# Optimization experiments

Hardware: AMD Instinct MI355X
Metric: run time of the kernel (lower is better)

## Reference

```python
import jax, jax.numpy as jnp
import numpy as np
from jax import lax

EPS = 1e-12  # torch F.normalize eps

def setup_inputs() -> dict:
    key = jax.random.key(0)
    k1, k2, k3, k4, k5 = jax.random.split(key, 5)
    N = 4194304
    L = 64
    return {
        "T": jax.random.normal(k1, (1,), dtype=jnp.float32),
        "closed_manifold": jax.random.normal(k2, (N, 2), dtype=jnp.float32),
        "Ws": jax.random.normal(k3, (L, 2, 2), dtype=jnp.float32) * 0.5,
        "bs": jax.random.normal(k4, (L, 2), dtype=jnp.float32) * 0.1,
        "final_W": jax.random.normal(k5, (2, 2), dtype=jnp.float32) * 0.5,
    }

def reference(T, closed_manifold, Ws, bs, final_W):
    # T is accepted but unused, exactly as in the original forward.
    def step(X, wb):
        W, b = wb                      # W: [2,2], b: [2]
        Y = X @ W.T + b                # linear: [N,2]
        A = jnp.tanh(Y)                # activation
        X = (A + Y) * 0.5              # residual averaging (skip_connections=True)
        return X, None
    X, _ = lax.scan(step, closed_manifold, (Ws, bs))
    X = X @ final_W.T                  # final bias-free linear
    # F.normalize(X, p=2, dim=1): row-wise unit vectors with eps clamp
    norm = jnp.sqrt(jnp.sum(X * X, axis=-1, keepdims=True))
    X = X / jnp.maximum(norm, EPS)
    return X
```

## Files before the change

### kernel.cpp

```cpp
#include <hip/hip_runtime.h>


#define KPT 8
#define BLOCK 256

__global__ __launch_bounds__(BLOCK) void nig_kernel(
    const float* __restrict__ X_in,
    const float* __restrict__ Ws,
    const float* __restrict__ bs,
    const float* __restrict__ fW,
    float* __restrict__ out,
    int M,
    int L)
{
    const int tid = blockIdx.x * blockDim.x + threadIdx.x;
    const int nthreads = gridDim.x * blockDim.x;

    const float4* __restrict__ in4 = (const float4*)X_in;
    float4* __restrict__ out4 = (float4*)out;

    float x0[KPT], x1[KPT];
    int idx4[KPT / 2];
    bool ok[KPT / 2];

    #pragma unroll
    for (int j = 0; j < KPT / 2; ++j) {
        idx4[j] = tid + j * nthreads;
        ok[j] = idx4[j] < M;
        float4 v = ok[j] ? in4[idx4[j]] : make_float4(0.f, 0.f, 0.f, 0.f);
        x0[2 * j]     = v.x; x1[2 * j]     = v.y;
        x0[2 * j + 1] = v.z; x1[2 * j + 1] = v.w;
    }

    const float C = 2.8853900817779268f;

    for (int l = 0; l < L; ++l) {
        const float4 w = ((const float4*)Ws)[l];
        const float2 b = ((const float2*)bs)[l];
        #pragma unroll
        for (int k = 0; k < KPT; ++k) {
            float y0 = fmaf(w.x, x0[k], fmaf(w.y, x1[k], b.x));
            float y1 = fmaf(w.z, x0[k], fmaf(w.w, x1[k], b.y));
            float e0 = __builtin_amdgcn_exp2f(y0 * C);
            float e1 = __builtin_amdgcn_exp2f(y1 * C);
            float r0 = __builtin_amdgcn_rcpf(e0 + 1.0f);
            float r1 = __builtin_amdgcn_rcpf(e1 + 1.0f);
            x0[k] = fmaf(0.5f, y0, 0.5f) - r0;
            x1[k] = fmaf(0.5f, y1, 0.5f) - r1;
        }
    }

    const float fw0 = fW[0], fw1 = fW[1], fw2 = fW[2], fw3 = fW[3];

    #pragma unroll
    for (int j = 0; j < KPT / 2; ++j) {
        if (!ok[j]) continue;
        float4 v;
        #pragma unroll
        for (int h = 0; h < 2; ++h) {
            const int k = 2 * j + h;
            float z0 = fmaf(fw0, x0[k], fw1 * x1[k]);
            float z1 = fmaf(fw2, x0[k], fw3 * x1[k]);
            float s  = fmaf(z0, z0, z1 * z1);
            float n  = __builtin_amdgcn_sqrtf(s);
            float inv = __builtin_amdgcn_rcpf(fmaxf(n, 1e-12f));
            float o0 = z0 * inv, o1 = z1 * inv;
            if (h == 0) { v.x = o0; v.y = o1; }
            else        { v.z = o0; v.w = o1; }
        }
        out4[idx4[j]] = v;
    }
}

extern "C" void kernel_launch(void* const* d_in, const int* in_sizes, int n_in,
                              void* d_out, int out_size, void* d_ws, size_t ws_size,
                              hipStream_t stream) {
    const float* X  = (const float*)d_in[1];
    const float* Ws = (const float*)d_in[2];
    const float* bs = (const float*)d_in[3];
    const float* fW = (const float*)d_in[4];
    float* out = (float*)d_out;

    const int L = in_sizes[2] / 4;
    const int M = in_sizes[1] / 4;
    const int threads = (M + (KPT / 2) - 1) / (KPT / 2);
    const int grid = (threads + BLOCK - 1) / BLOCK;

    nig_kernel<<<grid, BLOCK, 0, stream>>>(X, Ws, bs, fW, out, M, L);
}
```

Measured before the change: 209.6 us.

## Replace rcp-based tanh with polynomial in exp2, packed f2 math, scaled state

Keeps the layer state pre-scaled by 2*log2(e) so the per-layer multiply disappears, and computes tanh from exp2(-|y|) with a degree-6 polynomial for 1/(1+q) instead of a reciprocal, restoring the sign with copysign. Arithmetic is written on 2-wide float vectors so the compiler can emit packed FMA instructions, and the layer loop is unrolled by 4. This trades the transcendental rcp for several packed FMAs. The polynomial approximation adds a small accuracy error that accumulates over the 64 layers.

```diff
diff --git a/kernel.cpp b/kernel.cpp
--- a/kernel.cpp
+++ b/kernel.cpp
@@ -1,7 +1,9 @@
 #include <hip/hip_runtime.h>
 
 
-#define KPT 8
+typedef float f2 __attribute__((ext_vector_type(2)));
+
+#define NP 4
 #define BLOCK 256
 
 __global__ __launch_bounds__(BLOCK) void nig_kernel(
@@ -15,60 +17,77 @@
 {
     const int tid = blockIdx.x * blockDim.x + threadIdx.x;
     const int nthreads = gridDim.x * blockDim.x;
-
     const float4* __restrict__ in4 = (const float4*)X_in;
     float4* __restrict__ out4 = (float4*)out;
 
-    float x0[KPT], x1[KPT];
-    int idx4[KPT / 2];
-    bool ok[KPT / 2];
+    const float C     = 2.8853900817779268f;
+    const float halfC = 1.4426950408889634f;
 
+    f2 X0[NP], X1[NP];
+    int idx[NP]; bool ok[NP];
     #pragma unroll
-    for (int j = 0; j < KPT / 2; ++j) {
-        idx4[j] = tid + j * nthreads;
-        ok[j] = idx4[j] < M;
-        float4 v = ok[j] ? in4[idx4[j]] : make_float4(0.f, 0.f, 0.f, 0.f);
-        x0[2 * j]     = v.x; x1[2 * j]     = v.y;
-        x0[2 * j + 1] = v.z; x1[2 * j + 1] = v.w;
+    for (int j = 0; j < NP; ++j) {
+        idx[j] = tid + j * nthreads;
+        ok[j] = idx[j] < M;
+        float4 v = ok[j] ? in4[idx[j]] : make_float4(0.f, 0.f, 0.f, 0.f);
+        X0[j] = (f2){v.x, v.z} * C;
+        X1[j] = (f2){v.y, v.w} * C;
     }
 
-    const float C = 2.8853900817779268f;
+    const float p0 = 0.999992f,  p1 = -0.999210f, p2 = 0.986366f,
+                p3 = -0.907073f, p4 = 0.675347f,  p5 = -0.329296f,
+                p6 = 0.0738812f;
 
+    #pragma unroll 4
     for (int l = 0; l < L; ++l) {
         const float4 w = ((const float4*)Ws)[l];
         const float2 b = ((const float2*)bs)[l];
+        const float cb0 = C * b.x, cb1 = C * b.y;
         #pragma unroll
-        for (int k = 0; k < KPT; ++k) {
-            float y0 = fmaf(w.x, x0[k], fmaf(w.y, x1[k], b.x));
-            float y1 = fmaf(w.z, x0[k], fmaf(w.w, x1[k], b.y));
-            float e0 = __builtin_amdgcn_exp2f(y0 * C);
-            float e1 = __builtin_amdgcn_exp2f(y1 * C);
-            float r0 = __builtin_amdgcn_rcpf(e0 + 1.0f);
-            float r1 = __builtin_amdgcn_rcpf(e1 + 1.0f);
-            x0[k] = fmaf(0.5f, y0, 0.5f) - r0;
-            x1[k] = fmaf(0.5f, y1, 0.5f) - r1;
+        for (int j = 0; j < NP; ++j) {
+            f2 y0 = w.x * X0[j] + w.y * X1[j] + cb0;
+            f2 y1 = w.z * X0[j] + w.w * X1[j] + cb1;
+            f2 q0, q1;
+            q0.x = __builtin_amdgcn_exp2f(-__builtin_fabsf(y0.x));
+            q0.y = __builtin_amdgcn_exp2f(-__builtin_fabsf(y0.y));
+            q1.x = __builtin_amdgcn_exp2f(-__builtin_fabsf(y1.x));
+            q1.y = __builtin_amdgcn_exp2f(-__builtin_fabsf(y1.y));
+            f2 P0 = p6;
+            P0 = P0 * q0 + p5; P0 = P0 * q0 + p4; P0 = P0 * q0 + p3;
+            P0 = P0 * q0 + p2; P0 = P0 * q0 + p1; P0 = P0 * q0 + p0;
+            f2 P1 = p6;
+            P1 = P1 * q1 + p5; P1 = P1 * q1 + p4; P1 = P1 * q1 + p3;
+            P1 = P1 * q1 + p2; P1 = P1 * q1 + p1; P1 = P1 * q1 + p0;
+            f2 m0 = q0 * P0, m1 = q1 * P1;
+            f2 h0 = halfC - C * m0;
+            f2 h1 = halfC - C * m1;
+            f2 s0, s1;
+            s0.x = __builtin_copysignf(h0.x, y0.x);
+            s0.y = __builtin_copysignf(h0.y, y0.y);
+            s1.x = __builtin_copysignf(h1.x, y1.x);
+            s1.y = __builtin_copysignf(h1.y, y1.y);
+            X0[j] = 0.5f * y0 + s0;
+            X1[j] = 0.5f * y1 + s1;
         }
     }
 
-    const float fw0 = fW[0], fw1 = fW[1], fw2 = fW[2], fw3 = fW[3];
+    const float ic = 0.34657359027997264f;
+    const float g0 = fW[0] * ic, g1 = fW[1] * ic, g2 = fW[2] * ic, g3 = fW[3] * ic;
 
     #pragma unroll
-    for (int j = 0; j < KPT / 2; ++j) {
+    for (int j = 0; j < NP; ++j) {
         if (!ok[j]) continue;
-        float4 v;
-        #pragma unroll
-        for (int h = 0; h < 2; ++h) {
-            const int k = 2 * j + h;
-            float z0 = fmaf(fw0, x0[k], fw1 * x1[k]);
-            float z1 = fmaf(fw2, x0[k], fw3 * x1[k]);
-            float s  = fmaf(z0, z0, z1 * z1);
-            float n  = __builtin_amdgcn_sqrtf(s);
-            float inv = __builtin_amdgcn_rcpf(fmaxf(n, 1e-12f));
-            float o0 = z0 * inv, o1 = z1 * inv;
-            if (h == 0) { v.x = o0; v.y = o1; }
-            else        { v.z = o0; v.w = o1; }
-        }
-        out4[idx4[j]] = v;
+        f2 z0 = g0 * X0[j] + g1 * X1[j];
+        f2 z1 = g2 * X0[j] + g3 * X1[j];
+        f2 s  = z0 * z0 + z1 * z1;
+        float na = __builtin_amdgcn_sqrtf(s.x);
+        float nb = __builtin_amdgcn_sqrtf(s.y);
+        float ia = __builtin_amdgcn_rcpf(fmaxf(na, 1e-12f));
+        float ib = __builtin_amdgcn_rcpf(fmaxf(nb, 1e-12f));
+        float4 o;
+        o.x = z0.x * ia; o.y = z1.x * ia;
+        o.z = z0.y * ib; o.w = z1.y * ib;
+        out4[idx[j]] = o;
     }
 }
 
@@ -83,7 +102,7 @@
 
     const int L = in_sizes[2] / 4;
     const int M = in_sizes[1] / 4;
-    const int threads = (M + (KPT / 2) - 1) / (KPT / 2);
+    const int threads = (M + NP - 1) / NP;
     const int grid = (threads + BLOCK - 1) / BLOCK;
 
     nig_kernel<<<grid, BLOCK, 0, stream>>>(X, Ws, bs, fW, out, M, L);
```

Result: slower. 219.8 us (+4.8%).
